# Performance work log

Measured on AMD Instinct MI355X. Metric: run time of the kernel, lower is better.

The kernel has to match this reference:

```python
import jax, jax.numpy as jnp
import numpy as np

D_MODEL, D_K, D_V = 1024, 64, 64
B, S = 2, 4096
NEG = 1e9


def setup_inputs() -> dict:
    key = jax.random.key(0)
    ks = jax.random.split(key, 10)
    Q = jax.random.normal(ks[0], (B, S, D_MODEL), dtype=jnp.float32)
    K = jax.random.normal(ks[1], (B, S, D_MODEL), dtype=jnp.float32)
    V = jax.random.normal(ks[2], (B, S, D_MODEL), dtype=jnp.float32)
    mask = jax.random.randint(ks[3], (B, S, S), 0, 2, dtype=jnp.int32)
    sc = 1.0 / np.sqrt(D_MODEL)
    Wq = jax.random.normal(ks[4], (D_K, D_MODEL), dtype=jnp.float32) * sc
    bq = jnp.zeros((D_K,), dtype=jnp.float32)
    Wk = jax.random.normal(ks[5], (D_K, D_MODEL), dtype=jnp.float32) * sc
    bk = jnp.zeros((D_K,), dtype=jnp.float32)
    Wv = jax.random.normal(ks[6], (D_V, D_MODEL), dtype=jnp.float32) * sc
    bv = jnp.zeros((D_V,), dtype=jnp.float32)
    return {"Q": Q, "K": K, "V": V, "mask": mask,
            "Wq": Wq, "bq": bq, "Wk": Wk, "bk": bk, "Wv": Wv, "bv": bv}


def reference(Q, K, V, mask, Wq, bq, Wk, bk, Wv, bv):
    # Linear projections: q,k -> [B,S,d_k], v -> [B,S,d_v]
    q = jnp.einsum('bsm,km->bsk', Q, Wq) + bq
    k = jnp.einsum('bsm,km->bsk', K, Wk) + bk
    v = jnp.einsum('bsm,vm->bsv', V, Wv) + bv
    # Scaled dot-product scores [B,S,S]
    x = jnp.einsum('bqk,bsk->bqs', q, k) / jnp.sqrt(jnp.float32(D_K))
    m = mask.astype(x.dtype)
    x = x * m - NEG * (1.0 - m)
    x = jax.nn.softmax(x, axis=2)
    y = jnp.einsum('bqs,bsv->bqv', x, v)
    return y
```

## Files before the change

### kernel.cpp

```cpp
#include <hip/hip_runtime.h>

typedef unsigned short u16;
typedef unsigned long long u64;
typedef __bf16 bf16x8 __attribute__((ext_vector_type(8)));
typedef float f32x4 __attribute__((ext_vector_type(4)));

#define MFMA16(a, b, c) __builtin_amdgcn_mfma_f32_16x16x32_bf16((a), (b), (c), 0, 0, 0)

__device__ __forceinline__ bf16x8 ld8(const u16* p) {
    return *reinterpret_cast<const bf16x8*>(p);
}

__device__ __forceinline__ unsigned pk2(float a, float b) {
    unsigned short ua = __builtin_bit_cast(unsigned short, (__bf16)a);
    unsigned short ub = __builtin_bit_cast(unsigned short, (__bf16)b);
    return (unsigned)ua | ((unsigned)ub << 16);
}

__device__ __forceinline__ bf16x8 cvt8(float4 a, float4 b) {
    bf16x8 r;
    r[0] = (__bf16)a.x; r[1] = (__bf16)a.y; r[2] = (__bf16)a.z; r[3] = (__bf16)a.w;
    r[4] = (__bf16)b.x; r[5] = (__bf16)b.y; r[6] = (__bf16)b.z; r[7] = (__bf16)b.w;
    return r;
}

__global__ __launch_bounds__(256) void wcvt_kernel(
    const float* __restrict__ Wq, const float* __restrict__ Wk,
    const float* __restrict__ Wv, u16* __restrict__ wb)
{
    const int t = blockIdx.x * 256 + threadIdx.x;
    const int mat = t >> 13;
    const int idx = (t & 8191) * 8;
    const float* src = (mat == 0) ? Wq : (mat == 1) ? Wk : Wv;
    float4 a = *(const float4*)(src + idx);
    float4 b = *(const float4*)(src + idx + 4);
    uint4 o;
    o.x = pk2(a.x, a.y); o.y = pk2(a.z, a.w);
    o.z = pk2(b.x, b.y); o.w = pk2(b.z, b.w);
    *reinterpret_cast<uint4*>(wb + (size_t)mat * 65536 + idx) = o;
}

__global__ __launch_bounds__(256) void projpack_kernel(
    const float* __restrict__ Q, const float* __restrict__ K, const float* __restrict__ V,
    const float* __restrict__ bq, const float* __restrict__ bk, const float* __restrict__ bv,
    const u16* __restrict__ wb, const int* __restrict__ mask,
    u16* __restrict__ qb, u16* __restrict__ kb, u16* __restrict__ vtb,
    u64* __restrict__ bits64)
{
    const int lane = threadIdx.x & 63;
    const int w    = threadIdx.x >> 6;

    if (blockIdx.x >= 384) {
        const int gwv = (blockIdx.x - 384) * 4 + w;
        const int* mp = mask + (size_t)gwv * 4096 + lane;
        u64* op = bits64 + (size_t)gwv * 64;
        #pragma unroll 1
        for (int step = 0; step < 8; ++step) {
            const int* sp = mp + step * 512;
            const u64 b0 = __ballot(sp[0]   != 0);
            const u64 b1 = __ballot(sp[64]  != 0);
            const u64 b2 = __ballot(sp[128] != 0);
            const u64 b3 = __ballot(sp[192] != 0);
            const u64 b4 = __ballot(sp[256] != 0);
            const u64 b5 = __ballot(sp[320] != 0);
            const u64 b6 = __ballot(sp[384] != 0);
            const u64 b7 = __ballot(sp[448] != 0);
            u64 mine = b0;
            if (lane == 1) mine = b1;
            if (lane == 2) mine = b2;
            if (lane == 3) mine = b3;
            if (lane == 4) mine = b4;
            if (lane == 5) mine = b5;
            if (lane == 6) mine = b6;
            if (lane == 7) mine = b7;
            if (lane < 8) op[step * 8 + lane] = mine;
        }
        return;
    }

    const int mat  = blockIdx.x >> 7;
    const int tile = blockIdx.x & 127;
    const int c = lane & 15, g = lane >> 4;

    const float* X = (mat == 0) ? Q : (mat == 1) ? K : V;
    const u16*   W = wb + (size_t)mat * 65536;

    const int rw = tile * 64 + w * 16;
    const float* xp = X + (size_t)(rw + c) * 1024 + g * 8;
    const u16*   wp = W + (size_t)c * 1024 + g * 8;

    f32x4 acc[4] = {};
    float4 xa = *(const float4*)xp;
    float4 xb = *(const float4*)(xp + 4);

    #pragma unroll 2
    for (int kk = 0; kk < 32; ++kk) {
        bf16x8 a = cvt8(xa, xb);
        if (kk < 31) {
            xa = *(const float4*)(xp + (kk + 1) * 32);
            xb = *(const float4*)(xp + (kk + 1) * 32 + 4);
        }
        const u16* wk = wp + kk * 32;
        if (mat < 2) {
            #pragma unroll
            for (int t = 0; t < 4; ++t)
                acc[t] = MFMA16(a, ld8(wk + t * 16 * 1024), acc[t]);
        } else {
            #pragma unroll
            for (int t = 0; t < 4; ++t)
                acc[t] = MFMA16(ld8(wk + t * 16 * 1024), a, acc[t]);
        }
    }

    if (mat < 2) {
        const float* bias = (mat == 0) ? bq : bk;
        u16* dst = (mat == 0) ? qb : kb;
        #pragma unroll
        for (int t = 0; t < 4; ++t) {
            const float bz = bias[t * 16 + c];
            #pragma unroll
            for (int r = 0; r < 4; ++r) {
                const int row = rw + g * 4 + r;
                dst[(size_t)row * 64 + t * 16 + c] =
                    __builtin_bit_cast(u16, (__bf16)(acc[t][r] + bz));
            }
        }
    } else {
        const int sg = rw + c;
        const int bidx = sg >> 12, sin = sg & 4095;
        #pragma unroll
        for (int t = 0; t < 4; ++t) {
            #pragma unroll
            for (int r = 0; r < 4; ++r) {
                const int dv = t * 16 + g * 4 + r;
                vtb[(size_t)(bidx * 64 + dv) * 4096 + sin] =
                    __builtin_bit_cast(u16, (__bf16)(acc[t][r] + bv[dv]));
            }
        }
    }
}

__global__ __launch_bounds__(256) void attn_kernel(
    const unsigned* __restrict__ bits, const u16* __restrict__ qb,
    const u16* __restrict__ kb, const u16* __restrict__ vtb,
    float* __restrict__ pacc, float* __restrict__ pm, float* __restrict__ pl)
{
    __shared__ uint2 plds[4][128];
    const int lane = threadIdx.x & 63, w = threadIdx.x >> 6;
    const int c = lane & 15, g = lane >> 4;
    const int gw    = blockIdx.x * 4 + w;
    const int strip = gw >> 3;
    const int chunk = gw & 7;
    const int b     = strip >> 8;
    const int q0    = (strip & 255) * 16;
    const int sBase = chunk * 512;
    const float SSC = 0.18033688011112042f;

    const u16* qrow = qb + (size_t)((b << 12) + q0 + c) * 64 + g * 8;
    const bf16x8 qf0 = ld8(qrow);
    const bf16x8 qf1 = ld8(qrow + 32);

    const u16* kfp = kb  + (((size_t)b << 12) + sBase + c) * 64 + g * 8;
    const u16* vfp = vtb + (size_t)(b * 64 + c) * 4096 + sBase + g * 8;
    const unsigned* brow = bits + (size_t)((b << 12) + q0 + c) * 128 + (sBase >> 5);

    f32x4 acc0 = {}, acc1 = {}, acc2 = {}, acc3 = {};
    const f32x4 zf = {};
    float m_run = -__builtin_inff(), l_run = 0.f;

    unsigned wA = brow[0], wB = brow[1];
    bf16x8 k00 = ld8(kfp),            k01 = ld8(kfp + 32);
    bf16x8 k10 = ld8(kfp + 16 * 64),  k11 = ld8(kfp + 16 * 64 + 32);

    #pragma unroll 1
    for (int it = 0; it < 16; ++it) {
        const u16* vp = vfp + it * 32;
        const bf16x8 v0 = ld8(vp);
        const bf16x8 v1 = ld8(vp + 16 * 4096);
        const bf16x8 v2 = ld8(vp + 32 * 4096);
        const bf16x8 v3 = ld8(vp + 48 * 4096);

        f32x4 d0 = MFMA16(k00, qf0, zf);
        d0 = MFMA16(k01, qf1, d0);
        f32x4 d1 = MFMA16(k10, qf0, zf);
        d1 = MFMA16(k11, qf1, d1);

        const int no = (it < 15) ? (it + 1) * 2048 : it * 2048;
        k00 = ld8(kfp + no);            k01 = ld8(kfp + no + 32);
        k10 = ld8(kfp + no + 16 * 64);  k11 = ld8(kfp + no + 16 * 64 + 32);

        const unsigned wc_ = wA;
        wA = wB;
        wB = brow[(it + 2 < 16) ? (it + 2) : 15];

        const unsigned s0b = wc_ >> (g * 4);
        const unsigned s1b = wc_ >> (16 + g * 4);
        const float x0 = (s0b & 1u) ? d0[0] * SSC : -1e9f;
        const float x1 = (s0b & 2u) ? d0[1] * SSC : -1e9f;
        const float x2 = (s0b & 4u) ? d0[2] * SSC : -1e9f;
        const float x3 = (s0b & 8u) ? d0[3] * SSC : -1e9f;
        const float x4 = (s1b & 1u) ? d1[0] * SSC : -1e9f;
        const float x5 = (s1b & 2u) ? d1[1] * SSC : -1e9f;
        const float x6 = (s1b & 4u) ? d1[2] * SSC : -1e9f;
        const float x7 = (s1b & 8u) ? d1[3] * SSC : -1e9f;

        float tm = fmaxf(fmaxf(fmaxf(x0, x1), fmaxf(x2, x3)),
                         fmaxf(fmaxf(x4, x5), fmaxf(x6, x7)));
        tm = fmaxf(tm, __shfl_xor(tm, 16));
        tm = fmaxf(tm, __shfl_xor(tm, 32));
        const float m_new = fmaxf(m_run, tm);
        const float f = exp2f(m_run - m_new);

        const float p0 = exp2f(x0 - m_new), p1 = exp2f(x1 - m_new);
        const float p2 = exp2f(x2 - m_new), p3 = exp2f(x3 - m_new);
        const float p4 = exp2f(x4 - m_new), p5 = exp2f(x5 - m_new);
        const float p6 = exp2f(x6 - m_new), p7 = exp2f(x7 - m_new);
        float rs = ((p0 + p1) + (p2 + p3)) + ((p4 + p5) + (p6 + p7));
        rs += __shfl_xor(rs, 16);
        rs += __shfl_xor(rs, 32);
        l_run = l_run * f + rs;
        m_run = m_new;

        plds[w][c * 8 + ( g      ^ (c & 7))] = make_uint2(pk2(p0, p1), pk2(p2, p3));
        plds[w][c * 8 + ((g + 4) ^ (c & 7))] = make_uint2(pk2(p4, p5), pk2(p6, p7));

        if (__any(f < 1.0f)) {
            const float f0 = __shfl(f, g * 4 + 0);
            const float f1 = __shfl(f, g * 4 + 1);
            const float f2 = __shfl(f, g * 4 + 2);
            const float f3 = __shfl(f, g * 4 + 3);
            acc0[0] *= f0; acc0[1] *= f1; acc0[2] *= f2; acc0[3] *= f3;
            acc1[0] *= f0; acc1[1] *= f1; acc1[2] *= f2; acc1[3] *= f3;
            acc2[0] *= f0; acc2[1] *= f1; acc2[2] *= f2; acc2[3] *= f3;
            acc3[0] *= f0; acc3[1] *= f1; acc3[2] *= f2; acc3[3] *= f3;
        }

        union { uint2 u[2]; bf16x8 v; } pa;
        pa.u[0] = plds[w][c * 8 + ((2 * g    ) ^ (c & 7))];
        pa.u[1] = plds[w][c * 8 + ((2 * g + 1) ^ (c & 7))];

        acc0 = MFMA16(pa.v, v0, acc0);
        acc1 = MFMA16(pa.v, v1, acc1);
        acc2 = MFMA16(pa.v, v2, acc2);
        acc3 = MFMA16(pa.v, v3, acc3);
    }

    const size_t pidx = (size_t)(strip * 8 + chunk) * 16;
    #pragma unroll
    for (int r = 0; r < 4; ++r) {
        const size_t row = pidx + g * 4 + r;
        pacc[row * 64 +  0 + c] = acc0[r];
        pacc[row * 64 + 16 + c] = acc1[r];
        pacc[row * 64 + 32 + c] = acc2[r];
        pacc[row * 64 + 48 + c] = acc3[r];
    }
    if (lane < 16) {
        pm[pidx + c] = m_run;
        pl[pidx + c] = l_run;
    }
}

__global__ __launch_bounds__(256) void comb_kernel(
    const float* __restrict__ pacc, const float* __restrict__ pm,
    const float* __restrict__ pl, float* __restrict__ out)
{
    const int t = blockIdx.x * 256 + threadIdx.x;
    const int r = t >> 6, dv = t & 63;
    const int strip = r >> 4, qi = r & 15;
    const int base = strip * 128 + qi;
    float mv[8];
    float M = -__builtin_inff();
    #pragma unroll
    for (int cc = 0; cc < 8; ++cc) { mv[cc] = pm[base + cc * 16]; M = fmaxf(M, mv[cc]); }
    float num = 0.f, den = 0.f;
    #pragma unroll
    for (int cc = 0; cc < 8; ++cc) {
        const float wgt = exp2f(mv[cc] - M);
        num += wgt * pacc[(size_t)(base + cc * 16) * 64 + dv];
        den += wgt * pl[base + cc * 16];
    }
    out[t] = num / den;
}

extern "C" void kernel_launch(void* const* d_in, const int* in_sizes, int n_in,
                              void* d_out, int out_size, void* d_ws, size_t ws_size,
                              hipStream_t stream)
{
    const float* Q    = (const float*)d_in[0];
    const float* K    = (const float*)d_in[1];
    const float* V    = (const float*)d_in[2];
    const int*   mask = (const int*)d_in[3];
    const float* Wq   = (const float*)d_in[4];
    const float* bq   = (const float*)d_in[5];
    const float* Wk   = (const float*)d_in[6];
    const float* bk   = (const float*)d_in[7];
    const float* Wv   = (const float*)d_in[8];
    const float* bv   = (const float*)d_in[9];
    float* out = (float*)d_out;

    char* ws = (char*)d_ws;
    u16*   wb   = (u16*)(ws);
    u16*   qb   = (u16*)(ws + 393216);
    u16*   kb   = (u16*)(ws + 393216 + 1048576);
    u16*   vtb  = (u16*)(ws + 393216 + 2097152);
    u64*   bits = (u64*)(ws + 4194304);
    float* pm   = (float*)(ws + 8388608);
    float* pl   = (float*)(ws + 8388608 + 262144);
    float* pacc = (float*)(ws + 8388608 + 524288);

    wcvt_kernel<<<96, 256, 0, stream>>>(Wq, Wk, Wv, wb);
    projpack_kernel<<<2432, 256, 0, stream>>>(Q, K, V, bq, bk, bv, wb, mask,
                                              qb, kb, vtb, bits);
    attn_kernel<<<1024, 256, 0, stream>>>((const unsigned*)bits, qb, kb, vtb, pacc, pm, pl);
    comb_kernel<<<2048, 256, 0, stream>>>(pacc, pm, pl, out);
}
```

Measured before the change: 137.6 us.

## Repack mask bits with vectorized loads, split projection, deepen prefetch

Mask packing moves out of the projection kernel and is merged with the weight conversion into one kernel. It reads the int mask with 16-byte vector loads and a new strided bit layout, so the attention kernel loads each row's eight 64-bit words once and selects bits per lane. The projection kernel becomes standalone with launch bounds of one block and a register prefetch of eight K-steps ahead, aimed at hiding global-load latency. This adds register pressure and an extra launch boundary, and it changes the bit layout both producer and consumer depend on.

```diff
diff --git a/kernel.cpp b/kernel.cpp
--- a/kernel.cpp
+++ b/kernel.cpp
@@ -24,62 +24,69 @@
     return r;
 }
 
-__global__ __launch_bounds__(256) void wcvt_kernel(
+__global__ __launch_bounds__(256) void packcvt_kernel(
+    const int* __restrict__ mask, u64* __restrict__ bits,
     const float* __restrict__ Wq, const float* __restrict__ Wk,
     const float* __restrict__ Wv, u16* __restrict__ wb)
 {
-    const int t = blockIdx.x * 256 + threadIdx.x;
-    const int mat = t >> 13;
-    const int idx = (t & 8191) * 8;
-    const float* src = (mat == 0) ? Wq : (mat == 1) ? Wk : Wv;
-    float4 a = *(const float4*)(src + idx);
-    float4 b = *(const float4*)(src + idx + 4);
-    uint4 o;
-    o.x = pk2(a.x, a.y); o.y = pk2(a.z, a.w);
-    o.z = pk2(b.x, b.y); o.w = pk2(b.z, b.w);
-    *reinterpret_cast<uint4*>(wb + (size_t)mat * 65536 + idx) = o;
-}
-
-__global__ __launch_bounds__(256) void projpack_kernel(
+    if (blockIdx.x >= 2048) {
+        const int t = (blockIdx.x - 2048) * 256 + threadIdx.x;
+        const int mat = t >> 13;
+        const int idx = (t & 8191) * 8;
+        const float* src = (mat == 0) ? Wq : (mat == 1) ? Wk : Wv;
+        float4 a = *(const float4*)(src + idx);
+        float4 b = *(const float4*)(src + idx + 4);
+        uint4 o;
+        o.x = pk2(a.x, a.y); o.y = pk2(a.z, a.w);
+        o.z = pk2(b.x, b.y); o.w = pk2(b.z, b.w);
+        *reinterpret_cast<uint4*>(wb + (size_t)mat * 65536 + idx) = o;
+        return;
+    }
+
+    const int lane = threadIdx.x & 63, w = threadIdx.x >> 6;
+    const int row = blockIdx.x * 4 + w;
+    const int* mp = mask + (size_t)row * 4096 + lane * 4;
+    u64* op = bits + (size_t)row * 64;
+
+    int4 h0[8], h1[8];
+    #pragma unroll
+    for (int j = 0; j < 8; ++j) h0[j] = *(const int4*)(mp + j * 256);
+    #pragma unroll
+    for (int j = 0; j < 8; ++j) h1[j] = *(const int4*)(mp + 2048 + j * 256);
+
+    u64 mine0 = 0, mine1 = 0;
+    #pragma unroll
+    for (int j = 0; j < 8; ++j) {
+        const u64 b0 = __ballot(h0[j].x != 0);
+        const u64 b1 = __ballot(h0[j].y != 0);
+        const u64 b2 = __ballot(h0[j].z != 0);
+        const u64 b3 = __ballot(h0[j].w != 0);
+        if (lane == j * 4 + 0) mine0 = b0;
+        if (lane == j * 4 + 1) mine0 = b1;
+        if (lane == j * 4 + 2) mine0 = b2;
+        if (lane == j * 4 + 3) mine0 = b3;
+        const u64 c0 = __ballot(h1[j].x != 0);
+        const u64 c1 = __ballot(h1[j].y != 0);
+        const u64 c2 = __ballot(h1[j].z != 0);
+        const u64 c3 = __ballot(h1[j].w != 0);
+        if (lane == j * 4 + 0) mine1 = c0;
+        if (lane == j * 4 + 1) mine1 = c1;
+        if (lane == j * 4 + 2) mine1 = c2;
+        if (lane == j * 4 + 3) mine1 = c3;
+    }
+    if (lane < 32) { op[lane] = mine0; op[32 + lane] = mine1; }
+}
+
+__global__ __launch_bounds__(256, 1) void proj_kernel(
     const float* __restrict__ Q, const float* __restrict__ K, const float* __restrict__ V,
     const float* __restrict__ bq, const float* __restrict__ bk, const float* __restrict__ bv,
-    const u16* __restrict__ wb, const int* __restrict__ mask,
-    u16* __restrict__ qb, u16* __restrict__ kb, u16* __restrict__ vtb,
-    u64* __restrict__ bits64)
-{
+    const u16* __restrict__ wb, u16* __restrict__ qb, u16* __restrict__ kb,
+    u16* __restrict__ vtb)
+{
+    const int mat  = blockIdx.x >> 7;
+    const int tile = blockIdx.x & 127;
     const int lane = threadIdx.x & 63;
     const int w    = threadIdx.x >> 6;
-
-    if (blockIdx.x >= 384) {
-        const int gwv = (blockIdx.x - 384) * 4 + w;
-        const int* mp = mask + (size_t)gwv * 4096 + lane;
-        u64* op = bits64 + (size_t)gwv * 64;
-        #pragma unroll 1
-        for (int step = 0; step < 8; ++step) {
-            const int* sp = mp + step * 512;
-            const u64 b0 = __ballot(sp[0]   != 0);
-            const u64 b1 = __ballot(sp[64]  != 0);
-            const u64 b2 = __ballot(sp[128] != 0);
-            const u64 b3 = __ballot(sp[192] != 0);
-            const u64 b4 = __ballot(sp[256] != 0);
-            const u64 b5 = __ballot(sp[320] != 0);
-            const u64 b6 = __ballot(sp[384] != 0);
-            const u64 b7 = __ballot(sp[448] != 0);
-            u64 mine = b0;
-            if (lane == 1) mine = b1;
-            if (lane == 2) mine = b2;
-            if (lane == 3) mine = b3;
-            if (lane == 4) mine = b4;
-            if (lane == 5) mine = b5;
-            if (lane == 6) mine = b6;
-            if (lane == 7) mine = b7;
-            if (lane < 8) op[step * 8 + lane] = mine;
-        }
-        return;
-    }
-
-    const int mat  = blockIdx.x >> 7;
-    const int tile = blockIdx.x & 127;
     const int c = lane & 15, g = lane >> 4;
 
     const float* X = (mat == 0) ? Q : (mat == 1) ? K : V;
@@ -90,25 +97,33 @@
     const u16*   wp = W + (size_t)c * 1024 + g * 8;
 
     f32x4 acc[4] = {};
-    float4 xa = *(const float4*)xp;
-    float4 xb = *(const float4*)(xp + 4);
-
-    #pragma unroll 2
-    for (int kk = 0; kk < 32; ++kk) {
-        bf16x8 a = cvt8(xa, xb);
-        if (kk < 31) {
-            xa = *(const float4*)(xp + (kk + 1) * 32);
-            xb = *(const float4*)(xp + (kk + 1) * 32 + 4);
-        }
-        const u16* wk = wp + kk * 32;
-        if (mat < 2) {
-            #pragma unroll
-            for (int t = 0; t < 4; ++t)
-                acc[t] = MFMA16(a, ld8(wk + t * 16 * 1024), acc[t]);
-        } else {
-            #pragma unroll
-            for (int t = 0; t < 4; ++t)
-                acc[t] = MFMA16(ld8(wk + t * 16 * 1024), a, acc[t]);
+
+    float4 A[8], B[8];
+    #pragma unroll
+    for (int j = 0; j < 8; ++j) {
+        A[j] = *(const float4*)(xp + j * 32);
+        B[j] = *(const float4*)(xp + j * 32 + 4);
+    }
+
+    #pragma unroll 1
+    for (int kt = 0; kt < 4; ++kt) {
+        const int base  = kt * 8;
+        const int nbase = (kt < 3) ? base + 8 : base;
+        #pragma unroll
+        for (int j = 0; j < 8; ++j) {
+            const bf16x8 a = cvt8(A[j], B[j]);
+            A[j] = *(const float4*)(xp + (nbase + j) * 32);
+            B[j] = *(const float4*)(xp + (nbase + j) * 32 + 4);
+            const u16* wk = wp + (base + j) * 32;
+            if (mat < 2) {
+                #pragma unroll
+                for (int t = 0; t < 4; ++t)
+                    acc[t] = MFMA16(a, ld8(wk + t * 16384), acc[t]);
+            } else {
+                #pragma unroll
+                for (int t = 0; t < 4; ++t)
+                    acc[t] = MFMA16(ld8(wk + t * 16384), a, acc[t]);
+            }
         }
     }
 
@@ -141,7 +156,7 @@
 }
 
 __global__ __launch_bounds__(256) void attn_kernel(
-    const unsigned* __restrict__ bits, const u16* __restrict__ qb,
+    const u64* __restrict__ bits, const u16* __restrict__ qb,
     const u16* __restrict__ kb, const u16* __restrict__ vtb,
     float* __restrict__ pacc, float* __restrict__ pm, float* __restrict__ pl)
 {
@@ -162,87 +177,99 @@
 
     const u16* kfp = kb  + (((size_t)b << 12) + sBase + c) * 64 + g * 8;
     const u16* vfp = vtb + (size_t)(b * 64 + c) * 4096 + sBase + g * 8;
-    const unsigned* brow = bits + (size_t)((b << 12) + q0 + c) * 128 + (sBase >> 5);
+
+    const u64* bp = bits + (size_t)((b << 12) + q0 + c) * 64 + chunk * 8;
+    const u64 Wd0 = bp[0], Wd1 = bp[1], Wd2 = bp[2], Wd3 = bp[3];
+    const u64 Wd4 = bp[4], Wd5 = bp[5], Wd6 = bp[6], Wd7 = bp[7];
 
     f32x4 acc0 = {}, acc1 = {}, acc2 = {}, acc3 = {};
     const f32x4 zf = {};
     float m_run = -__builtin_inff(), l_run = 0.f;
 
-    unsigned wA = brow[0], wB = brow[1];
     bf16x8 k00 = ld8(kfp),            k01 = ld8(kfp + 32);
     bf16x8 k10 = ld8(kfp + 16 * 64),  k11 = ld8(kfp + 16 * 64 + 32);
 
-    #pragma unroll 1
-    for (int it = 0; it < 16; ++it) {
-        const u16* vp = vfp + it * 32;
-        const bf16x8 v0 = ld8(vp);
-        const bf16x8 v1 = ld8(vp + 16 * 4096);
-        const bf16x8 v2 = ld8(vp + 32 * 4096);
-        const bf16x8 v3 = ld8(vp + 48 * 4096);
-
-        f32x4 d0 = MFMA16(k00, qf0, zf);
-        d0 = MFMA16(k01, qf1, d0);
-        f32x4 d1 = MFMA16(k10, qf0, zf);
-        d1 = MFMA16(k11, qf1, d1);
-
-        const int no = (it < 15) ? (it + 1) * 2048 : it * 2048;
-        k00 = ld8(kfp + no);            k01 = ld8(kfp + no + 32);
-        k10 = ld8(kfp + no + 16 * 64);  k11 = ld8(kfp + no + 16 * 64 + 32);
-
-        const unsigned wc_ = wA;
-        wA = wB;
-        wB = brow[(it + 2 < 16) ? (it + 2) : 15];
-
-        const unsigned s0b = wc_ >> (g * 4);
-        const unsigned s1b = wc_ >> (16 + g * 4);
-        const float x0 = (s0b & 1u) ? d0[0] * SSC : -1e9f;
-        const float x1 = (s0b & 2u) ? d0[1] * SSC : -1e9f;
-        const float x2 = (s0b & 4u) ? d0[2] * SSC : -1e9f;
-        const float x3 = (s0b & 8u) ? d0[3] * SSC : -1e9f;
-        const float x4 = (s1b & 1u) ? d1[0] * SSC : -1e9f;
-        const float x5 = (s1b & 2u) ? d1[1] * SSC : -1e9f;
-        const float x6 = (s1b & 4u) ? d1[2] * SSC : -1e9f;
-        const float x7 = (s1b & 8u) ? d1[3] * SSC : -1e9f;
-
-        float tm = fmaxf(fmaxf(fmaxf(x0, x1), fmaxf(x2, x3)),
-                         fmaxf(fmaxf(x4, x5), fmaxf(x6, x7)));
-        tm = fmaxf(tm, __shfl_xor(tm, 16));
-        tm = fmaxf(tm, __shfl_xor(tm, 32));
-        const float m_new = fmaxf(m_run, tm);
-        const float f = exp2f(m_run - m_new);
-
-        const float p0 = exp2f(x0 - m_new), p1 = exp2f(x1 - m_new);
-        const float p2 = exp2f(x2 - m_new), p3 = exp2f(x3 - m_new);
-        const float p4 = exp2f(x4 - m_new), p5 = exp2f(x5 - m_new);
-        const float p6 = exp2f(x6 - m_new), p7 = exp2f(x7 - m_new);
-        float rs = ((p0 + p1) + (p2 + p3)) + ((p4 + p5) + (p6 + p7));
-        rs += __shfl_xor(rs, 16);
-        rs += __shfl_xor(rs, 32);
-        l_run = l_run * f + rs;
-        m_run = m_new;
-
-        plds[w][c * 8 + ( g      ^ (c & 7))] = make_uint2(pk2(p0, p1), pk2(p2, p3));
-        plds[w][c * 8 + ((g + 4) ^ (c & 7))] = make_uint2(pk2(p4, p5), pk2(p6, p7));
-
-        if (__any(f < 1.0f)) {
-            const float f0 = __shfl(f, g * 4 + 0);
-            const float f1 = __shfl(f, g * 4 + 1);
-            const float f2 = __shfl(f, g * 4 + 2);
-            const float f3 = __shfl(f, g * 4 + 3);
-            acc0[0] *= f0; acc0[1] *= f1; acc0[2] *= f2; acc0[3] *= f3;
-            acc1[0] *= f0; acc1[1] *= f1; acc1[2] *= f2; acc1[3] *= f3;
-            acc2[0] *= f0; acc2[1] *= f1; acc2[2] *= f2; acc2[3] *= f3;
-            acc3[0] *= f0; acc3[1] *= f1; acc3[2] *= f2; acc3[3] *= f3;
+    #pragma unroll
+    for (int half = 0; half < 2; ++half) {
+        const u64 Wr0 = half ? Wd4 : Wd0;
+        const u64 Wr1 = half ? Wd5 : Wd1;
+        const u64 Wr2 = half ? Wd6 : Wd2;
+        const u64 Wr3 = half ? Wd7 : Wd3;
+        #pragma unroll 1
+        for (int it2 = 0; it2 < 8; ++it2) {
+            const int it = half * 8 + it2;
+            const int s0 = sBase + it * 32;
+
+            const u16* vp = vfp + it * 32;
+            const bf16x8 v0 = ld8(vp);
+            const bf16x8 v1 = ld8(vp + 16 * 4096);
+            const bf16x8 v2 = ld8(vp + 32 * 4096);
+            const bf16x8 v3 = ld8(vp + 48 * 4096);
+
+            f32x4 d0 = MFMA16(k00, qf0, zf);
+            d0 = MFMA16(k01, qf1, d0);
+            f32x4 d1 = MFMA16(k10, qf0, zf);
+            d1 = MFMA16(k11, qf1, d1);
+
+            const int no = (it < 15) ? (it + 1) * 2048 : it * 2048;
+            k00 = ld8(kfp + no);            k01 = ld8(kfp + no + 32);
+            k10 = ld8(kfp + no + 16 * 64);  k11 = ld8(kfp + no + 16 * 64 + 32);
+
+            const int sh = it2 * 8 + g;
+            const unsigned t0 = (unsigned)(Wr0 >> sh);
+            const unsigned t1 = (unsigned)(Wr1 >> sh);
+            const unsigned t2 = (unsigned)(Wr2 >> sh);
+            const unsigned t3 = (unsigned)(Wr3 >> sh);
+
+            const float x0 = (t0 & 1u)  ? d0[0] * SSC : -1e9f;
+            const float x1 = (t1 & 1u)  ? d0[1] * SSC : -1e9f;
+            const float x2 = (t2 & 1u)  ? d0[2] * SSC : -1e9f;
+            const float x3 = (t3 & 1u)  ? d0[3] * SSC : -1e9f;
+            const float x4 = (t0 & 16u) ? d1[0] * SSC : -1e9f;
+            const float x5 = (t1 & 16u) ? d1[1] * SSC : -1e9f;
+            const float x6 = (t2 & 16u) ? d1[2] * SSC : -1e9f;
+            const float x7 = (t3 & 16u) ? d1[3] * SSC : -1e9f;
+
+            float tm = fmaxf(fmaxf(fmaxf(x0, x1), fmaxf(x2, x3)),
+                             fmaxf(fmaxf(x4, x5), fmaxf(x6, x7)));
+            tm = fmaxf(tm, __shfl_xor(tm, 16));
+            tm = fmaxf(tm, __shfl_xor(tm, 32));
+            const float m_new = fmaxf(m_run, tm);
+            const float f = exp2f(m_run - m_new);
+
+            const float p0 = exp2f(x0 - m_new), p1 = exp2f(x1 - m_new);
+            const float p2 = exp2f(x2 - m_new), p3 = exp2f(x3 - m_new);
+            const float p4 = exp2f(x4 - m_new), p5 = exp2f(x5 - m_new);
+            const float p6 = exp2f(x6 - m_new), p7 = exp2f(x7 - m_new);
+            float rs = ((p0 + p1) + (p2 + p3)) + ((p4 + p5) + (p6 + p7));
+            rs += __shfl_xor(rs, 16);
+            rs += __shfl_xor(rs, 32);
+            l_run = l_run * f + rs;
+            m_run = m_new;
+
+            plds[w][c * 8 + ( g      ^ (c & 7))] = make_uint2(pk2(p0, p1), pk2(p2, p3));
+            plds[w][c * 8 + ((g + 4) ^ (c & 7))] = make_uint2(pk2(p4, p5), pk2(p6, p7));
+
+            if (__any(f < 1.0f)) {
+                const float f0 = __shfl(f, g * 4 + 0);
+                const float f1 = __shfl(f, g * 4 + 1);
+                const float f2 = __shfl(f, g * 4 + 2);
+                const float f3 = __shfl(f, g * 4 + 3);
+                acc0[0] *= f0; acc0[1] *= f1; acc0[2] *= f2; acc0[3] *= f3;
+                acc1[0] *= f0; acc1[1] *= f1; acc1[2] *= f2; acc1[3] *= f3;
+                acc2[0] *= f0; acc2[1] *= f1; acc2[2] *= f2; acc2[3] *= f3;
+                acc3[0] *= f0; acc3[1] *= f1; acc3[2] *= f2; acc3[3] *= f3;
+            }
+
+            union { uint2 u[2]; bf16x8 v; } pa;
+            pa.u[0] = plds[w][c * 8 + ((2 * g    ) ^ (c & 7))];
+            pa.u[1] = plds[w][c * 8 + ((2 * g + 1) ^ (c & 7))];
+
+            acc0 = MFMA16(pa.v, v0, acc0);
+            acc1 = MFMA16(pa.v, v1, acc1);
+            acc2 = MFMA16(pa.v, v2, acc2);
+            acc3 = MFMA16(pa.v, v3, acc3);
         }
-
-        union { uint2 u[2]; bf16x8 v; } pa;
-        pa.u[0] = plds[w][c * 8 + ((2 * g    ) ^ (c & 7))];
-        pa.u[1] = plds[w][c * 8 + ((2 * g + 1) ^ (c & 7))];
-
-        acc0 = MFMA16(pa.v, v0, acc0);
-        acc1 = MFMA16(pa.v, v1, acc1);
-        acc2 = MFMA16(pa.v, v2, acc2);
-        acc3 = MFMA16(pa.v, v3, acc3);
     }
 
     const size_t pidx = (size_t)(strip * 8 + chunk) * 16;
@@ -308,9 +335,8 @@
     float* pl   = (float*)(ws + 8388608 + 262144);
     float* pacc = (float*)(ws + 8388608 + 524288);
 
-    wcvt_kernel<<<96, 256, 0, stream>>>(Wq, Wk, Wv, wb);
-    projpack_kernel<<<2432, 256, 0, stream>>>(Q, K, V, bq, bk, bv, wb, mask,
-                                              qb, kb, vtb, bits);
-    attn_kernel<<<1024, 256, 0, stream>>>((const unsigned*)bits, qb, kb, vtb, pacc, pm, pl);
+    packcvt_kernel<<<2144, 256, 0, stream>>>(mask, bits, Wq, Wk, Wv, wb);
+    proj_kernel<<<384, 256, 0, stream>>>(Q, K, V, bq, bk, bv, wb, qb, kb, vtb);
+    attn_kernel<<<1024, 256, 0, stream>>>(bits, qb, kb, vtb, pacc, pm, pl);
     comb_kernel<<<2048, 256, 0, stream>>>(pacc, pm, pl, out);
 }
```

Result: slower. 145.5 us (+5.7%).
